# Performance work log

Measured on AMD Instinct MI355X. Metric: run time of the kernel, lower is better.

The kernel has to match this reference:

```python
import jax, jax.numpy as jnp
from jax import lax
import numpy as np

B, T, N = 32, 1024, 128


def setup_inputs() -> dict:
    key = jax.random.key(0)
    k1, k2, k3 = jax.random.split(key, 3)
    x = jax.random.normal(k1, (B, T, N), dtype=jnp.float32)
    w_init = jax.random.normal(k2, (B, N, N), dtype=jnp.float32)
    mask = jax.random.randint(k3, (B, T), 0, 2, dtype=jnp.int32)
    alpha = jnp.float32(0.9)
    eta = jnp.float32(0.01)
    return {"x": x, "w_init": w_init, "alpha": alpha, "eta": eta, "mask": mask}


def reference(x, w_init, alpha, eta, mask):
    # x: (B,T,N), w_init: (B,N,N), mask: (B,T) int {0,1}
    maskf = mask.astype(x.dtype)

    def step(w, inp):
        xt, mt = inp                       # (B,N), (B,)
        yt = jnp.einsum('bij,bj->bi', w, xt)           # read-out with OLD w
        outer = xt[:, :, None] * xt[:, None, :]        # (B,N,N) Hebbian outer product
        w_new = alpha * w + eta * outer                # decay + Hebbian update
        m = mt[:, None, None]
        w = m * w_new + (1.0 - m) * w                  # masked update
        return w, yt

    xs = jnp.swapaxes(x, 0, 1)     # (T,B,N)
    ms = jnp.swapaxes(maskf, 0, 1) # (T,B)
    w_final, ys = lax.scan(step, w_init, (xs, ms))
    y_seq = jnp.swapaxes(ys, 0, 1)  # (B,T,N)
    return w_final, y_seq
```

## Files before the change

### kernel.cpp

```cpp
#include <hip/hip_runtime.h>

#define BB 32
#define TT 1024
#define NN 128
#define YB 256

#define ROR_ADD(p, ctrl)                                                      \
  p += __int_as_float(__builtin_amdgcn_update_dpp(                            \
      0, __float_as_int(p), ctrl, 0xF, 0xF, true));

__global__ __launch_bounds__(128)
void bdh_seq_kernel(const float* __restrict__ x,
                    const float* __restrict__ w_init,
                    const float* __restrict__ alpha_p,
                    const float* __restrict__ eta_p,
                    const int*   __restrict__ mask,
                    float* __restrict__ out)
{
    const int tid  = threadIdx.x;
    const int bidx = blockIdx.x;
    const int b      = bidx & 31;
    const int i_base = (bidx >> 5) << 3;
    const int wv     = tid >> 6;
    const int lane   = tid & 63;
    const int rr     = lane >> 4;
    const int i      = i_base + (wv << 2) + rr;
    const int j0     = (lane & 15) << 3;

    __shared__ int   mbuf[TT];
    __shared__ float Cbuf[TT];
    __shared__ float Sbuf[TT];
    __shared__ float Rbuf[TT / 16];
    __shared__ float ybuf[YB][8];

    const float alpha = alpha_p[0];
    const float eta   = eta_p[0];
    const float rcp_a = 1.0f / alpha;

    const float* xb = x + (size_t)b * TT * NN;
    const int*   mb = mask + b * TT;
    float* yout = out + (size_t)BB * NN * NN + (size_t)b * TT * NN;

    {
        int4*       mv = (int4*)mbuf;
        const int4* mg = (const int4*)mb;
        mv[tid]       = mg[tid];
        mv[tid + 128] = mg[tid + 128];
    }
    __syncthreads();
    if (tid < 64) {
        float e_prev = eta;
        float e      = eta;
#pragma unroll
        for (int k = 0; k < 16; ++k) {
            const int m = mbuf[tid * 16 + k];
            e = m ? e * rcp_a : e;
            Cbuf[tid * 16 + k] = m ? e : 0.0f;
            Sbuf[tid * 16 + k] = eta / e_prev;
            e_prev = e;
        }
        Rbuf[tid] = eta / e;
    }
    __syncthreads();

    const float* wrow = w_init + ((size_t)b * NN + i) * NN + j0;
    float4 v0 = *reinterpret_cast<const float4*>(wrow);
    float4 v1 = *reinterpret_cast<const float4*>(wrow + 4);

    float4 Xc0[8], Xc1[8], Xn0[8], Xn1[8];
    float  xic[8], xin[8];
    float  Cc[16];
    float  p[16];
    float  Rg;

#define LOADG(X0, X1, XI, tbase)                                              \
  {                                                                           \
    const float* gp = xb + (size_t)(tbase) * NN;                              \
    _Pragma("unroll")                                                         \
    for (int k = 0; k < 8; ++k) {                                             \
      X0[k] = *reinterpret_cast<const float4*>(gp + k * NN + j0);             \
      X1[k] = *reinterpret_cast<const float4*>(gp + k * NN + j0 + 4);         \
      XI[k] = gp[k * NN + i];                                                 \
    }                                                                         \
  }

#define LOADC(tbase)                                                          \
  {                                                                           \
    _Pragma("unroll")                                                         \
    for (int q = 0; q < 4; ++q)                                               \
      *reinterpret_cast<float4*>(&Cc[q * 4]) =                                \
          *reinterpret_cast<const float4*>(&Cbuf[(tbase) + q * 4]);           \
  }

#define COMPG(X0, X1, XI, cbase, pbase)                                       \
  {                                                                           \
    _Pragma("unroll")                                                         \
    for (int k = 0; k < 8; ++k) {                                             \
      const float ci = Cc[(cbase) + k] * XI[k];                               \
      float d = v0.x * X0[k].x;                                               \
      d = fmaf(v0.y, X0[k].y, d);                                             \
      d = fmaf(v0.z, X0[k].z, d);                                             \
      d = fmaf(v0.w, X0[k].w, d);                                             \
      d = fmaf(v1.x, X1[k].x, d);                                             \
      d = fmaf(v1.y, X1[k].y, d);                                             \
      d = fmaf(v1.z, X1[k].z, d);                                             \
      d = fmaf(v1.w, X1[k].w, d);                                             \
      p[(pbase) + k] = d;                                                     \
      v0.x = fmaf(ci, X0[k].x, v0.x);                                         \
      v0.y = fmaf(ci, X0[k].y, v0.y);                                         \
      v0.z = fmaf(ci, X0[k].z, v0.z);                                         \
      v0.w = fmaf(ci, X0[k].w, v0.w);                                         \
      v1.x = fmaf(ci, X1[k].x, v1.x);                                         \
      v1.y = fmaf(ci, X1[k].y, v1.y);                                         \
      v1.z = fmaf(ci, X1[k].z, v1.z);                                         \
      v1.w = fmaf(ci, X1[k].w, v1.w);                                         \
    }                                                                         \
  }

    LOADG(Xc0, Xc1, xic, 0);
    LOADG(Xn0, Xn1, xin, 8);
    LOADC(0);
    Rg = Rbuf[0];

#pragma unroll 1
    for (int t = 0; t < TT; t += 16) {
        COMPG(Xc0, Xc1, xic, 0, 0);
        if (t + 16 < TT) { LOADG(Xc0, Xc1, xic, t + 16); }
        COMPG(Xn0, Xn1, xin, 8, 8);
        if (t + 24 < TT) { LOADG(Xn0, Xn1, xin, t + 24); }

        v0.x *= Rg; v0.y *= Rg; v0.z *= Rg; v0.w *= Rg;
        v1.x *= Rg; v1.y *= Rg; v1.z *= Rg; v1.w *= Rg;

        if (t + 16 < TT) { LOADC(t + 16); Rg = Rbuf[(t >> 4) + 1]; }

#pragma unroll
        for (int k = 0; k < 16; ++k) { ROR_ADD(p[k], 0x121); }
#pragma unroll
        for (int k = 0; k < 16; ++k) { ROR_ADD(p[k], 0x122); }
#pragma unroll
        for (int k = 0; k < 16; ++k) { ROR_ADD(p[k], 0x124); }
#pragma unroll
        for (int k = 0; k < 16; ++k) { ROR_ADD(p[k], 0x128); }

        if ((lane & 15) == 0) {
#pragma unroll
            for (int k = 0; k < 16; ++k)
                ybuf[(t + k) & (YB - 1)][(wv << 2) + rr] = p[k];
        }

        if (((t + 16) & (YB - 1)) == 0) {
            __syncthreads();
            const int t0 = t + 16 - YB;
#pragma unroll
            for (int pass = 0; pass < 16; ++pass) {
                const int idx = (pass << 7) + tid;
                const int tq  = idx >> 3;
                const int il  = idx & 7;
                yout[(size_t)(t0 + tq) * NN + i_base + il] =
                    ybuf[tq][il] * Sbuf[t0 + tq];
            }
            __syncthreads();
        }
    }
#undef LOADG
#undef LOADC
#undef COMPG

    float* wout = out + ((size_t)b * NN + i) * NN + j0;
    *reinterpret_cast<float4*>(wout)     = v0;
    *reinterpret_cast<float4*>(wout + 4) = v1;
}

extern "C" void kernel_launch(void* const* d_in, const int* in_sizes, int n_in,
                              void* d_out, int out_size, void* d_ws, size_t ws_size,
                              hipStream_t stream)
{
    const float* x      = (const float*)d_in[0];
    const float* w_init = (const float*)d_in[1];
    const float* alpha  = (const float*)d_in[2];
    const float* eta    = (const float*)d_in[3];
    const int*   mask   = (const int*)d_in[4];
    float*       out    = (float*)d_out;

    dim3 grid(512), block(128);
    hipLaunchKernelGGL(bdh_seq_kernel, grid, block, 0, stream,
                       x, w_init, alpha, eta, mask, out);
}
```

Baseline: 207.1 us.

## Halve per-thread row slice and double block size for more parallelism

Each thread now owns 4 columns of a W row instead of 8, with 32 threads per row and 256 threads per block, so each block covers the same 8 rows with twice as many threads. The row reduction gains an extra DPP row-broadcast step to sum across 32 lanes, and lane 16 writes the result. This halves the per-thread serial FMA chain and the register footprint, at the cost of twice the redundant x loads per block and an extra cross-row reduction stage.

```diff
diff --git a/kernel.cpp b/kernel.cpp
--- a/kernel.cpp
+++ b/kernel.cpp
@@ -8,8 +8,9 @@
 #define ROR_ADD(p, ctrl)                                                      \
   p += __int_as_float(__builtin_amdgcn_update_dpp(                            \
       0, __float_as_int(p), ctrl, 0xF, 0xF, true));
+#define BCAST15_ADD(p) ROR_ADD(p, 0x142)
 
-__global__ __launch_bounds__(128)
+__global__ __launch_bounds__(256)
 void bdh_seq_kernel(const float* __restrict__ x,
                     const float* __restrict__ w_init,
                     const float* __restrict__ alpha_p,
@@ -21,11 +22,10 @@
     const int bidx = blockIdx.x;
     const int b      = bidx & 31;
     const int i_base = (bidx >> 5) << 3;
-    const int wv     = tid >> 6;
-    const int lane   = tid & 63;
-    const int rr     = lane >> 4;
-    const int i      = i_base + (wv << 2) + rr;
-    const int j0     = (lane & 15) << 3;
+    const int rloc   = tid >> 5;
+    const int i      = i_base + rloc;
+    const int cg     = tid & 31;
+    const int j0     = cg << 2;
 
     __shared__ int   mbuf[TT];
     __shared__ float Cbuf[TT];
@@ -41,12 +41,7 @@
     const int*   mb = mask + b * TT;
     float* yout = out + (size_t)BB * NN * NN + (size_t)b * TT * NN;
 
-    {
-        int4*       mv = (int4*)mbuf;
-        const int4* mg = (const int4*)mb;
-        mv[tid]       = mg[tid];
-        mv[tid + 128] = mg[tid + 128];
-    }
+    ((int4*)mbuf)[tid] = ((const int4*)mb)[tid];
     __syncthreads();
     if (tid < 64) {
         float e_prev = eta;
@@ -63,23 +58,21 @@
     }
     __syncthreads();
 
-    const float* wrow = w_init + ((size_t)b * NN + i) * NN + j0;
-    float4 v0 = *reinterpret_cast<const float4*>(wrow);
-    float4 v1 = *reinterpret_cast<const float4*>(wrow + 4);
+    float4 v = *reinterpret_cast<const float4*>(
+        w_init + ((size_t)b * NN + i) * NN + j0);
 
-    float4 Xc0[8], Xc1[8], Xn0[8], Xn1[8];
+    float4 Xc[8], Xn[8];
     float  xic[8], xin[8];
     float  Cc[16];
     float  p[16];
     float  Rg;
 
-#define LOADG(X0, X1, XI, tbase)                                              \
+#define LOADG(X, XI, tbase)                                                   \
   {                                                                           \
     const float* gp = xb + (size_t)(tbase) * NN;                              \
     _Pragma("unroll")                                                         \
     for (int k = 0; k < 8; ++k) {                                             \
-      X0[k] = *reinterpret_cast<const float4*>(gp + k * NN + j0);             \
-      X1[k] = *reinterpret_cast<const float4*>(gp + k * NN + j0 + 4);         \
+      X[k]  = *reinterpret_cast<const float4*>(gp + k * NN + j0);             \
       XI[k] = gp[k * NN + i];                                                 \
     }                                                                         \
   }
@@ -92,46 +85,36 @@
           *reinterpret_cast<const float4*>(&Cbuf[(tbase) + q * 4]);           \
   }
 
-#define COMPG(X0, X1, XI, cbase, pbase)                                       \
+#define COMPG(X, XI, cbase, pbase)                                            \
   {                                                                           \
     _Pragma("unroll")                                                         \
     for (int k = 0; k < 8; ++k) {                                             \
       const float ci = Cc[(cbase) + k] * XI[k];                               \
-      float d = v0.x * X0[k].x;                                               \
-      d = fmaf(v0.y, X0[k].y, d);                                             \
-      d = fmaf(v0.z, X0[k].z, d);                                             \
-      d = fmaf(v0.w, X0[k].w, d);                                             \
-      d = fmaf(v1.x, X1[k].x, d);                                             \
-      d = fmaf(v1.y, X1[k].y, d);                                             \
-      d = fmaf(v1.z, X1[k].z, d);                                             \
-      d = fmaf(v1.w, X1[k].w, d);                                             \
+      float d = v.x * X[k].x;                                                 \
+      d = fmaf(v.y, X[k].y, d);                                               \
+      d = fmaf(v.z, X[k].z, d);                                               \
+      d = fmaf(v.w, X[k].w, d);                                               \
       p[(pbase) + k] = d;                                                     \
-      v0.x = fmaf(ci, X0[k].x, v0.x);                                         \
-      v0.y = fmaf(ci, X0[k].y, v0.y);                                         \
-      v0.z = fmaf(ci, X0[k].z, v0.z);                                         \
-      v0.w = fmaf(ci, X0[k].w, v0.w);                                         \
-      v1.x = fmaf(ci, X1[k].x, v1.x);                                         \
-      v1.y = fmaf(ci, X1[k].y, v1.y);                                         \
-      v1.z = fmaf(ci, X1[k].z, v1.z);                                         \
-      v1.w = fmaf(ci, X1[k].w, v1.w);                                         \
+      v.x = fmaf(ci, X[k].x, v.x);                                            \
+      v.y = fmaf(ci, X[k].y, v.y);                                            \
+      v.z = fmaf(ci, X[k].z, v.z);                                            \
+      v.w = fmaf(ci, X[k].w, v.w);                                            \
     }                                                                         \
   }
 
-    LOADG(Xc0, Xc1, xic, 0);
-    LOADG(Xn0, Xn1, xin, 8);
+    LOADG(Xc, xic, 0);
+    LOADG(Xn, xin, 8);
     LOADC(0);
     Rg = Rbuf[0];
 
 #pragma unroll 1
     for (int t = 0; t < TT; t += 16) {
-        COMPG(Xc0, Xc1, xic, 0, 0);
-        if (t + 16 < TT) { LOADG(Xc0, Xc1, xic, t + 16); }
-        COMPG(Xn0, Xn1, xin, 8, 8);
-        if (t + 24 < TT) { LOADG(Xn0, Xn1, xin, t + 24); }
+        COMPG(Xc, xic, 0, 0);
+        if (t + 16 < TT) { LOADG(Xc, xic, t + 16); }
+        COMPG(Xn, xin, 8, 8);
+        if (t + 24 < TT) { LOADG(Xn, xin, t + 24); }
 
-        v0.x *= Rg; v0.y *= Rg; v0.z *= Rg; v0.w *= Rg;
-        v1.x *= Rg; v1.y *= Rg; v1.z *= Rg; v1.w *= Rg;
-
+        v.x *= Rg; v.y *= Rg; v.z *= Rg; v.w *= Rg;
         if (t + 16 < TT) { LOADC(t + 16); Rg = Rbuf[(t >> 4) + 1]; }
 
 #pragma unroll
@@ -142,19 +125,21 @@
         for (int k = 0; k < 16; ++k) { ROR_ADD(p[k], 0x124); }
 #pragma unroll
         for (int k = 0; k < 16; ++k) { ROR_ADD(p[k], 0x128); }
+#pragma unroll
+        for (int k = 0; k < 16; ++k) { BCAST15_ADD(p[k]); }
 
-        if ((lane & 15) == 0) {
+        if (cg == 16) {
 #pragma unroll
             for (int k = 0; k < 16; ++k)
-                ybuf[(t + k) & (YB - 1)][(wv << 2) + rr] = p[k];
+                ybuf[(t + k) & (YB - 1)][rloc] = p[k];
         }
 
         if (((t + 16) & (YB - 1)) == 0) {
             __syncthreads();
             const int t0 = t + 16 - YB;
 #pragma unroll
-            for (int pass = 0; pass < 16; ++pass) {
-                const int idx = (pass << 7) + tid;
+            for (int pass = 0; pass < 8; ++pass) {
+                const int idx = (pass << 8) + tid;
                 const int tq  = idx >> 3;
                 const int il  = idx & 7;
                 yout[(size_t)(t0 + tq) * NN + i_base + il] =
@@ -168,8 +153,7 @@
 #undef COMPG
 
     float* wout = out + ((size_t)b * NN + i) * NN + j0;
-    *reinterpret_cast<float4*>(wout)     = v0;
-    *reinterpret_cast<float4*>(wout + 4) = v1;
+    *reinterpret_cast<float4*>(wout) = v;
 }
 
 extern "C" void kernel_launch(void* const* d_in, const int* in_sizes, int n_in,
@@ -183,7 +167,7 @@
     const int*   mask   = (const int*)d_in[4];
     float*       out    = (float*)d_out;
 
-    dim3 grid(512), block(128);
+    dim3 grid(512), block(256);
     hipLaunchKernelGGL(bdh_seq_kernel, grid, block, 0, stream,
                        x, w_init, alpha, eta, mask, out);
 }
```

New measurement: 236.3 us. 14.1% more time.
